# Optimization experiments

Hardware: AMD Instinct MI355X
Metric: run time of the kernel (lower is better)

Reference implementation:

```python
import jax, jax.numpy as jnp
import numpy as np

RADIUS = 0.1
NSAMPLE = 32
STRIDE = 4
EPS = 1e-5


def fps(p, M):
    # Furthest point sampling. p: [B, N, 3] -> idx [B, M] int32. First point is index 0.
    B, N, _ = p.shape

    def body(carry, _):
        dmin, last = carry
        lp = jnp.take_along_axis(p, last[:, None, None], axis=1)  # [B,1,3]
        d = jnp.sum((p - lp) ** 2, axis=-1)                       # [B,N]
        dmin = jnp.minimum(dmin, d)
        nxt = jnp.argmax(dmin, axis=-1).astype(jnp.int32)
        return (dmin, nxt), nxt

    first = jnp.zeros((B,), jnp.int32)
    dmin0 = jnp.full((B, N), jnp.inf, p.dtype)
    _, rest = jax.lax.scan(body, (dmin0, first), None, length=M - 1)
    return jnp.concatenate([first[None, :], rest], axis=0).T  # [B,M]


def ball_query(new_p, p, radius, K):
    # For each query, first K support indices with dist < radius (CUDA ballquery semantics:
    # pad with first found index; 0 if none). new_p [B,M,3], p [B,N,3] -> [B,M,K] int32.
    N = p.shape[1]
    d2 = (jnp.sum(new_p ** 2, -1)[:, :, None] + jnp.sum(p ** 2, -1)[:, None, :]
          - 2.0 * jnp.einsum('bmd,bnd->bmn', new_p, p))  # [B,M,N]
    scores = jnp.where(d2 < radius * radius,
                       jnp.arange(N, dtype=jnp.int32)[None, None, :], N)
    neg_vals, _ = jax.lax.top_k(-scores, K)  # K smallest scores, ascending
    idx = -neg_vals
    first = jnp.where(idx[..., :1] >= N, 0, idx[..., :1])
    return jnp.where(idx >= N, first, idx)


def bn(x, g, b):
    # BatchNorm (training-mode batch stats) over all dims except channel dim 1.
    axes = tuple(i for i in range(x.ndim) if i != 1)
    m = jnp.mean(x, axes, keepdims=True)
    v = jnp.var(x, axes, keepdims=True)
    shape = (1, -1) + (1,) * (x.ndim - 2)
    return g.reshape(shape) * (x - m) * jax.lax.rsqrt(v + EPS) + b.reshape(shape)


def setup_inputs() -> dict:
    key = jax.random.key(0)
    ks = jax.random.split(key, 6)
    B, N, C = 4, 8192, 64
    return {
        'p': jax.random.uniform(ks[0], (B, N, 3), jnp.float32),
        'f': jax.random.normal(ks[1], (B, C, N), jnp.float32),
        'w1': jax.random.normal(ks[2], (64, 3 + C), jnp.float32) * 0.05,
        'g1': jnp.ones((64,), jnp.float32),
        'b1': jnp.zeros((64,), jnp.float32),
        'w2': jax.random.normal(ks[3], (128, 64), jnp.float32) * 0.05,
        'g2': jnp.ones((128,), jnp.float32),
        'b2': jnp.zeros((128,), jnp.float32),
        'w_skip': jax.random.normal(ks[4], (128, C), jnp.float32) * 0.05,
        'b_skip': jnp.zeros((128,), jnp.float32),
    }


def reference(p, f, w1, g1, b1, w2, g2, b2, w_skip, b_skip):
    B, N, _ = p.shape
    C = f.shape[1]
    M = N // STRIDE
    idx = fps(p, M)                                                # [B,M]
    new_p = jnp.take_along_axis(p, idx[:, :, None], axis=1)        # [B,M,3]
    # residual branch: gather sampled features, 1x1 conv1d skip
    fi = jnp.take_along_axis(f, jnp.broadcast_to(idx[:, None, :], (B, C, M)), axis=2)
    identity = jnp.einsum('oc,bcm->bom', w_skip, fi) + b_skip[None, :, None]
    # ball-query grouping
    nidx = ball_query(new_p, p, RADIUS, NSAMPLE)                   # [B,M,K]
    flat = nidx.reshape(B, 1, M * NSAMPLE)
    pj = jnp.take_along_axis(p.transpose(0, 2, 1),
                             jnp.broadcast_to(flat, (B, 3, M * NSAMPLE)),
                             axis=2).reshape(B, 3, M, NSAMPLE)
    dp = pj - new_p.transpose(0, 2, 1)[:, :, :, None]              # [B,3,M,K]
    fj = jnp.take_along_axis(f, jnp.broadcast_to(flat, (B, C, M * NSAMPLE)),
                             axis=2).reshape(B, C, M, NSAMPLE)
    x = jnp.concatenate([dp, fj], axis=1)                          # [B,3+C,M,K]
    # conv-bn-relu, conv-bn (last block no act because use_res)
    x = jax.nn.relu(bn(jnp.einsum('oc,bcmk->bomk', w1, x), g1, b1))
    x = bn(jnp.einsum('oc,bcmk->bomk', w2, x), g2, b2)
    fout = jnp.max(x, axis=-1)                                     # [B,128,M]
    fout = jax.nn.relu(fout + identity)
    return new_p, fout, idx
```

## Files before the change

### kernel.cpp

```cpp
#include <hip/hip_runtime.h>
#include <math.h>

#define BB 4
#define NP 8192
#define CF 64
#define MQ 2048
#define KS 32

#define WS_G      0u
#define WS_NIDX   2097152u
#define WS_IDXI   2359296u
#define WS_ST1    2367488u
#define WS_ST2    2375680u
#define WS_SC1    2392064u
#define WS_SC2    2392192u
#define WS_MAXY2  2392448u

typedef float v2f __attribute__((ext_vector_type(2)));

#define FPS_T 256
#define FPS_NK 16

template <int CTRL>
__device__ __forceinline__ unsigned long long dpp_max_step(unsigned long long k) {
  int lo = (int)(unsigned)k;
  int hi = (int)(unsigned)(k >> 32);
  int slo = __builtin_amdgcn_update_dpp(0, lo, CTRL, 0xF, 0xF, true);
  int shi = __builtin_amdgcn_update_dpp(0, hi, CTRL, 0xF, 0xF, true);
  unsigned long long s =
      ((unsigned long long)(unsigned)shi << 32) | (unsigned long long)(unsigned)slo;
  return s > k ? s : k;
}

__global__ __launch_bounds__(256, 1) void fps_fused_kernel(
    const float* __restrict__ p, float* __restrict__ out, int* __restrict__ idx_i,
    const float* __restrict__ f, float* __restrict__ gout,
    const float* __restrict__ w1) {
#pragma clang fp contract(off)
  __shared__ __align__(16) char smem[NP * 16 + MQ * 4 + 2 * 4 * 8];
  int bx = blockIdx.x;
  int t = threadIdx.x;

  if (bx >= 4) {
    float (*tile)[65] = (float (*)[65])smem;
    float (*wlds)[68] = (float (*)[68])(smem + 16640);
    float* plds = (float*)(smem + 16640 + 17408);
    int tb = bx - 4;
    int b = tb >> 7;
    int n0 = (tb & 127) * 64;
    int cc = t >> 6;
    int nn = t & 63;
    #pragma unroll
    for (int r = 0; r < 16; ++r) {
      int c = cc * 16 + r;
      tile[c][nn] = f[((size_t)b * 64 + c) * NP + n0 + nn];
    }
    for (int i = t; i < 64 * 67; i += 256) {
      wlds[i / 67][i % 67] = w1[i];
    }
    if (t < 192) plds[t] = p[((size_t)b * NP + n0) * 3 + t];
    __syncthreads();
    int wv = t >> 6, lane = t & 63;
    float wreg[67];
    #pragma unroll
    for (int c = 0; c < 67; ++c) wreg[c] = wlds[lane][c];
    for (int q = 0; q < 16; ++q) {
      int pt = wv * 16 + q;
      float acc = wreg[0] * plds[pt * 3 + 0];
      acc += wreg[1] * plds[pt * 3 + 1];
      acc += wreg[2] * plds[pt * 3 + 2];
      #pragma unroll
      for (int c = 0; c < 64; ++c) acc += wreg[3 + c] * tile[c][pt];
      gout[((size_t)b * NP + n0 + pt) * 64 + lane] = acc;
    }
    return;
  }

  float4* sp4 = (float4*)smem;
  int* win = (int*)(smem + NP * 16);
  unsigned long long* wkey = (unsigned long long*)(smem + NP * 16 + MQ * 4);

  int b = bx;
  const float* pb = p + (size_t)b * NP * 3;
  float* out_newp = out;
  float* out_idxf = out + BB*MQ*3 + (size_t)BB*128*MQ;

  v2f px2[FPS_NK], py2[FPS_NK], pz2[FPS_NK];
  float dmn0[FPS_NK], dmn1[FPS_NK];
  #pragma unroll
  for (int k = 0; k < FPS_NK; ++k) {
    int i0 = (2*k) * FPS_T + t;
    int i1 = i0 + FPS_T;
    float x0 = pb[i0*3+0], y0 = pb[i0*3+1], z0 = pb[i0*3+2];
    float x1 = pb[i1*3+0], y1 = pb[i1*3+1], z1 = pb[i1*3+2];
    px2[k] = (v2f){x0, x1}; py2[k] = (v2f){y0, y1}; pz2[k] = (v2f){z0, z1};
    sp4[i0] = make_float4(x0, y0, z0, 0.0f);
    sp4[i1] = make_float4(x1, y1, z1, 0.0f);
    dmn0[k] = INFINITY; dmn1[k] = INFINITY;
  }
  if (t == 0) win[0] = 0;
  __syncthreads();
  float lx = sp4[0].x, ly = sp4[0].y, lz = sp4[0].z;
  unsigned nt = ~(unsigned)t;

  for (int j = 1; j < MQ; ++j) {
#pragma clang fp contract(off)
    v2f l2x = (v2f){lx, lx}, l2y = (v2f){ly, ly}, l2z = (v2f){lz, lz};
    float bv0 = -1.0f, bv1 = -1.0f;
    unsigned bk0 = 0u, bk1 = 0u;
    #pragma unroll
    for (int k = 0; k < FPS_NK; ++k) {
      v2f dx = px2[k] - l2x;
      v2f dy = py2[k] - l2y;
      v2f dz = pz2[k] - l2z;
      v2f dd = ((dx*dx) + (dy*dy)) + (dz*dz);
      float m0 = fminf(dmn0[k], dd.x);  dmn0[k] = m0;
      float m1 = fminf(dmn1[k], dd.y);  dmn1[k] = m1;
      bool g0 = m0 > bv0;
      bv0 = g0 ? m0 : bv0;
      bk0 = g0 ? (unsigned)k : bk0;
      bool g1 = m1 > bv1;
      bv1 = g1 ? m1 : bv1;
      bk1 = g1 ? (unsigned)k : bk1;
    }
    unsigned bn0 = nt - (bk0 << 9);
    unsigned bn1 = nt - (bk1 << 9) - 256u;
    unsigned long long k0 =
        ((unsigned long long)__float_as_uint(bv0) << 32) | (unsigned long long)bn0;
    unsigned long long k1 =
        ((unsigned long long)__float_as_uint(bv1) << 32) | (unsigned long long)bn1;
    unsigned long long key = k0 > k1 ? k0 : k1;
    key = dpp_max_step<0x111>(key);
    key = dpp_max_step<0x112>(key);
    key = dpp_max_step<0x114>(key);
    key = dpp_max_step<0x118>(key);
    key = dpp_max_step<0x142>(key);
    key = dpp_max_step<0x143>(key);
    if ((t & 63) == 63) wkey[(j & 1) * 4 + (t >> 6)] = key;
    __syncthreads();
    const ulonglong2* wk2 = (const ulonglong2*)(&wkey[(j & 1) * 4]);
    ulonglong2 ka = wk2[0];
    ulonglong2 kb = wk2[1];
    unsigned long long m0 = ka.x > ka.y ? ka.x : ka.y;
    unsigned long long m1 = kb.x > kb.y ? kb.x : kb.y;
    unsigned long long kw = m0 > m1 ? m0 : m1;
    int wi = (int)(~(unsigned)kw);
    float4 c = sp4[wi];
    lx = c.x; ly = c.y; lz = c.z;
    if (t == 0) win[j] = wi;
  }

  __syncthreads();
  #pragma unroll
  for (int k = 0; k < MQ / FPS_T; ++k) {
    int j = k * FPS_T + t;
    int wi = win[j];
    out_idxf[b*MQ + j] = (float)wi;
    idx_i[b*MQ + j] = wi;
    float4 c = sp4[wi];
    float* np_ = &out_newp[(size_t)(b*MQ + j) * 3];
    np_[0] = c.x; np_[1] = c.y; np_[2] = c.z;
  }
}

__global__ __launch_bounds__(256) void ballq_kernel(
    const float* __restrict__ p, const float* __restrict__ newp,
    int* __restrict__ nidx) {
  int qid = blockIdx.x * 4 + (threadIdx.x >> 6);
  int lane = threadIdx.x & 63;
  int b = qid >> 11;
  const float* pb = p + (size_t)b * NP * 3;
  float qx = newp[qid*3], qy = newp[qid*3+1], qz = newp[qid*3+2];
  float sq_q = __fadd_rn(__fadd_rn(__fmul_rn(qx,qx), __fmul_rn(qy,qy)), __fmul_rn(qz,qz));
  const float R2 = (float)(0.1 * 0.1);
  int found = 0, first = -1;
  int* outp = nidx + (size_t)qid * KS;
  for (int base = 0; base < NP; base += 64) {
    int n = base + lane;
    float x = pb[n*3], y = pb[n*3+1], z = pb[n*3+2];
    float sq_p = __fadd_rn(__fadd_rn(__fmul_rn(x,x), __fmul_rn(y,y)), __fmul_rn(z,z));
    float dot  = __fadd_rn(__fadd_rn(__fmul_rn(qx,x), __fmul_rn(qy,y)), __fmul_rn(qz,z));
    float d2   = __fadd_rn(__fadd_rn(sq_q, sq_p), __fmul_rn(-2.0f, dot));
    bool hit = d2 < R2;
    unsigned long long mask = __ballot(hit);
    if (mask) {
      if (first < 0) first = base + __builtin_ctzll(mask);
      int cnt = __popcll(mask);
      if (found < KS) {
        int rank = __popcll(mask & ((1ull << lane) - 1ull));
        if (hit && found + rank < KS) outp[found + rank] = n;
      }
      found += cnt;
      if (found >= KS) break;
    }
  }
  int fcl = found < KS ? found : KS;
  int padv = first < 0 ? 0 : first;
  if (lane >= fcl && lane < KS) outp[lane] = padv;
}

__global__ __launch_bounds__(256) void p1_kernel(
    const float* __restrict__ g, const float* __restrict__ newp,
    const float* __restrict__ w1, const int* __restrict__ nidx,
    float* __restrict__ stats1) {
  __shared__ float wbs[4][64], wbq[4][64];
  int wv = threadIdx.x >> 6, lane = threadIdx.x & 63;
  int qid = blockIdx.x * 4 + wv;
  int b = qid >> 11;
  int nv = (lane < KS) ? nidx[(size_t)qid * KS + lane] : 0;
  float qx = newp[qid*3], qy = newp[qid*3+1], qz = newp[qid*3+2];
  float w0 = w1[lane*67+0], w1c = w1[lane*67+1], w2c = w1[lane*67+2];
  float hq = w0*qx + w1c*qy + w2c*qz;
  float ss = 0.f, qq = 0.f;
  for (int kb = 0; kb < KS; kb += 8) {
    float gv[8];
    #pragma unroll
    for (int u = 0; u < 8; ++u) {
      int n = __shfl(nv, kb + u);
      gv[u] = g[((size_t)b * NP + n) * 64 + lane];
    }
    #pragma unroll
    for (int u = 0; u < 8; ++u) {
      float a = gv[u] - hq;
      ss += a; qq += a * a;
    }
  }
  wbs[wv][lane] = ss; wbq[wv][lane] = qq;
  __syncthreads();
  if (threadIdx.x < 64) {
    float s  = wbs[0][threadIdx.x] + wbs[1][threadIdx.x] + wbs[2][threadIdx.x] + wbs[3][threadIdx.x];
    float s2 = wbq[0][threadIdx.x] + wbq[1][threadIdx.x] + wbq[2][threadIdx.x] + wbq[3][threadIdx.x];
    int slice = blockIdx.x & 63;
    atomicAdd(&stats1[(slice*2+0)*64 + threadIdx.x], s);
    atomicAdd(&stats1[(slice*2+1)*64 + threadIdx.x], s2);
  }
}

__global__ void fin1_kernel(const float* __restrict__ stats1,
                            const float* __restrict__ g, const float* __restrict__ bb,
                            float* __restrict__ sc) {
  int o = threadIdx.x;
  float s = 0.f, q = 0.f;
  for (int sl = 0; sl < 64; ++sl) { s += stats1[(sl*2+0)*64+o]; q += stats1[(sl*2+1)*64+o]; }
  const float cnt = (float)(BB * MQ * KS);
  float mean = s / cnt;
  float var = q / cnt - mean * mean;
  float rstd = 1.0f / sqrtf(var + 1e-5f);
  float gs = g[o] * rstd;
  sc[o] = gs;
  sc[64+o] = bb[o] - mean * gs;
}

__global__ void fin2_kernel(const float* __restrict__ stats2,
                            const float* __restrict__ g, const float* __restrict__ bb,
                            float* __restrict__ sc) {
  int o = threadIdx.x;
  float s = 0.f, q = 0.f;
  for (int sl = 0; sl < 64; ++sl) { s += stats2[(sl*2+0)*128+o]; q += stats2[(sl*2+1)*128+o]; }
  const float cnt = (float)(BB * MQ * KS);
  float mean = s / cnt;
  float var = q / cnt - mean * mean;
  float rstd = 1.0f / sqrtf(var + 1e-5f);
  float gs = g[o] * rstd;
  sc[o] = gs;
  sc[128+o] = bb[o] - mean * gs;
}

__global__ __launch_bounds__(256) void p2_kernel(
    const float* __restrict__ g, const float* __restrict__ newp,
    const float* __restrict__ w1, const float* __restrict__ w2,
    const int* __restrict__ nidx, const float* __restrict__ sc1,
    float* __restrict__ stats2, float* __restrict__ maxy2) {
  __shared__ __align__(16) float xbuf[4][KS][68];
  __shared__ float wbs[4][128], wbq[4][128];
  int wv = threadIdx.x >> 6, lane = threadIdx.x & 63;
  int qid = blockIdx.x * 4 + wv;
  int b = qid >> 11;
  int nv = (lane < KS) ? nidx[(size_t)qid * KS + lane] : 0;
  float qx = newp[qid*3], qy = newp[qid*3+1], qz = newp[qid*3+2];
  float w0 = w1[lane*67+0], w1c = w1[lane*67+1], w2c = w1[lane*67+2];
  float hq = w0*qx + w1c*qy + w2c*qz;
  float s1v = sc1[lane], t1v = sc1[64 + lane];
  for (int kb = 0; kb < KS; kb += 8) {
    float gv[8];
    #pragma unroll
    for (int u = 0; u < 8; ++u) {
      int n = __shfl(nv, kb + u);
      gv[u] = g[((size_t)b * NP + n) * 64 + lane];
    }
    #pragma unroll
    for (int u = 0; u < 8; ++u) {
      float a = gv[u] - hq;
      float h = fmaxf(0.0f, fmaf(a, s1v, t1v));
      xbuf[wv][kb + u][lane] = h;
    }
  }
  __syncthreads();
  const float4* w2a = (const float4*)(w2 + (size_t)lane * 64);
  const float4* w2b = (const float4*)(w2 + (size_t)(lane + 64) * 64);
  float4 wra[16], wrb[16];
  #pragma unroll
  for (int c4 = 0; c4 < 16; ++c4) { wra[c4] = w2a[c4]; wrb[c4] = w2b[c4]; }
  float ss0 = 0.f, qq0 = 0.f, mx0 = -INFINITY;
  float ss1 = 0.f, qq1 = 0.f, mx1 = -INFINITY;
  for (int kk = 0; kk < KS; ++kk) {
    const float4* hr = (const float4*)(&xbuf[wv][kk][0]);
    float a0 = 0.f, a1 = 0.f;
    #pragma unroll
    for (int c4 = 0; c4 < 16; ++c4) {
      float4 h4 = hr[c4];
      float4 wa = wra[c4]; float4 wb = wrb[c4];
      a0 += wa.x*h4.x + wa.y*h4.y + wa.z*h4.z + wa.w*h4.w;
      a1 += wb.x*h4.x + wb.y*h4.y + wb.z*h4.z + wb.w*h4.w;
    }
    ss0 += a0; qq0 += a0*a0; mx0 = fmaxf(mx0, a0);
    ss1 += a1; qq1 += a1*a1; mx1 = fmaxf(mx1, a1);
  }
  maxy2[(size_t)qid * 128 + lane] = mx0;
  maxy2[(size_t)qid * 128 + 64 + lane] = mx1;
  wbs[wv][lane] = ss0; wbs[wv][64+lane] = ss1;
  wbq[wv][lane] = qq0; wbq[wv][64+lane] = qq1;
  __syncthreads();
  if (threadIdx.x < 128) {
    float s  = wbs[0][threadIdx.x] + wbs[1][threadIdx.x] + wbs[2][threadIdx.x] + wbs[3][threadIdx.x];
    float s2 = wbq[0][threadIdx.x] + wbq[1][threadIdx.x] + wbq[2][threadIdx.x] + wbq[3][threadIdx.x];
    int slice = blockIdx.x & 63;
    atomicAdd(&stats2[(slice*2+0)*128 + threadIdx.x], s);
    atomicAdd(&stats2[(slice*2+1)*128 + threadIdx.x], s2);
  }
}

__global__ __launch_bounds__(256) void p3_kernel(
    const float* __restrict__ f, const int* __restrict__ idx_i,
    const float* __restrict__ w_skip, const float* __restrict__ b_skip,
    const float* __restrict__ sc2, const float* __restrict__ maxy2,
    float* __restrict__ outf) {
  __shared__ __align__(16) float flds[4][64];
  int wv = threadIdx.x >> 6, lane = threadIdx.x & 63;
  int qid = blockIdx.x * 4 + wv;
  int b = qid >> 11, m = qid & (MQ - 1);
  int n = idx_i[qid];
  flds[wv][lane] = f[((size_t)b * 64 + lane) * NP + n];
  const float4* f4 = (const float4*)(&flds[wv][0]);
  const float4* wa = (const float4*)(w_skip + (size_t)lane * 64);
  const float4* wb = (const float4*)(w_skip + (size_t)(lane + 64) * 64);
  float a0 = b_skip[lane], a1 = b_skip[lane + 64];
  #pragma unroll
  for (int c4 = 0; c4 < 16; ++c4) {
    float4 x = f4[c4]; float4 u = wa[c4]; float4 v = wb[c4];
    a0 += u.x*x.x + u.y*x.y + u.z*x.z + u.w*x.w;
    a1 += v.x*x.x + v.y*x.y + v.z*x.z + v.w*x.w;
  }
  float v0 = maxy2[(size_t)qid * 128 + lane];
  float v1 = maxy2[(size_t)qid * 128 + 64 + lane];
  float r0 = fmaxf(0.0f, fmaf(v0, sc2[lane],      sc2[128 + lane])      + a0);
  float r1 = fmaxf(0.0f, fmaf(v1, sc2[lane + 64], sc2[128 + lane + 64]) + a1);
  outf[((size_t)b * 128 + lane) * MQ + m] = r0;
  outf[((size_t)b * 128 + lane + 64) * MQ + m] = r1;
}

extern "C" void kernel_launch(void* const* d_in, const int* in_sizes, int n_in,
                              void* d_out, int out_size, void* d_ws, size_t ws_size,
                              hipStream_t stream) {
  (void)in_sizes; (void)n_in; (void)out_size; (void)ws_size;
  const float* p   = (const float*)d_in[0];
  const float* f   = (const float*)d_in[1];
  const float* w1  = (const float*)d_in[2];
  const float* g1  = (const float*)d_in[3];
  const float* b1  = (const float*)d_in[4];
  const float* w2  = (const float*)d_in[5];
  const float* g2  = (const float*)d_in[6];
  const float* b2  = (const float*)d_in[7];
  const float* wsk = (const float*)d_in[8];
  const float* bsk = (const float*)d_in[9];
  float* out = (float*)d_out;
  float* wsf = (float*)d_ws;

  float* gbuf  = wsf + WS_G;
  int*   nidx  = (int*)(wsf + WS_NIDX);
  int*   idxi  = (int*)(wsf + WS_IDXI);
  float* st1   = wsf + WS_ST1;
  float* st2   = wsf + WS_ST2;
  float* sc1   = wsf + WS_SC1;
  float* sc2   = wsf + WS_SC2;
  float* maxy2 = wsf + WS_MAXY2;

  float* out_newp = out;
  float* out_f    = out + BB*MQ*3;

  (void)hipMemsetAsync(st1, 0, (8192 + 16384) * sizeof(float), stream);

  fps_fused_kernel<<<4 + 512, FPS_T, 0, stream>>>(p, out, idxi, f, gbuf, w1);
  ballq_kernel<<<BB*MQ/4, 256, 0, stream>>>(p, out_newp, nidx);
  p1_kernel<<<BB*MQ/4, 256, 0, stream>>>(gbuf, out_newp, w1, nidx, st1);
  fin1_kernel<<<1, 64, 0, stream>>>(st1, g1, b1, sc1);
  p2_kernel<<<BB*MQ/4, 256, 0, stream>>>(gbuf, out_newp, w1, w2, nidx, sc1, st2, maxy2);
  fin2_kernel<<<1, 128, 0, stream>>>(st2, g2, b2, sc2);
  p3_kernel<<<BB*MQ/4, 256, 0, stream>>>(f, idxi, wsk, bsk, sc2, maxy2, out_f);
}
```

Measured before the change: 1.906 ms.

## Fold BN finalize into consumer kernels, prefetch ball-query points, pad LDS weight rows

Result: no change. 1.914 ms (+0.4%).

```diff
diff --git a/kernel.cpp b/kernel.cpp
--- a/kernel.cpp
+++ b/kernel.cpp
@@ -12,8 +12,6 @@
 #define WS_IDXI   2359296u
 #define WS_ST1    2367488u
 #define WS_ST2    2375680u
-#define WS_SC1    2392064u
-#define WS_SC2    2392192u
 #define WS_MAXY2  2392448u
 
 typedef float v2f __attribute__((ext_vector_type(2)));
@@ -43,8 +41,8 @@
 
   if (bx >= 4) {
     float (*tile)[65] = (float (*)[65])smem;
-    float (*wlds)[68] = (float (*)[68])(smem + 16640);
-    float* plds = (float*)(smem + 16640 + 17408);
+    float (*wlds)[69] = (float (*)[69])(smem + 16640);
+    float* plds = (float*)(smem + 16640 + 17664);
     int tb = bx - 4;
     int b = tb >> 7;
     int n0 = (tb & 127) * 64;
@@ -175,9 +173,11 @@
   const float R2 = (float)(0.1 * 0.1);
   int found = 0, first = -1;
   int* outp = nidx + (size_t)qid * KS;
+  float x = pb[lane*3], y = pb[lane*3+1], z = pb[lane*3+2];
   for (int base = 0; base < NP; base += 64) {
+    int nf = (base + 64 < NP) ? (base + 64 + lane) : lane;
+    float xn = pb[nf*3], yn = pb[nf*3+1], zn = pb[nf*3+2];
     int n = base + lane;
-    float x = pb[n*3], y = pb[n*3+1], z = pb[n*3+2];
     float sq_p = __fadd_rn(__fadd_rn(__fmul_rn(x,x), __fmul_rn(y,y)), __fmul_rn(z,z));
     float dot  = __fadd_rn(__fadd_rn(__fmul_rn(qx,x), __fmul_rn(qy,y)), __fmul_rn(qz,z));
     float d2   = __fadd_rn(__fadd_rn(sq_q, sq_p), __fmul_rn(-2.0f, dot));
@@ -193,6 +193,7 @@
       found += cnt;
       if (found >= KS) break;
     }
+    x = xn; y = yn; z = zn;
   }
   int fcl = found < KS ? found : KS;
   int padv = first < 0 ? 0 : first;
@@ -236,51 +237,39 @@
   }
 }
 
-__global__ void fin1_kernel(const float* __restrict__ stats1,
-                            const float* __restrict__ g, const float* __restrict__ bb,
-                            float* __restrict__ sc) {
-  int o = threadIdx.x;
-  float s = 0.f, q = 0.f;
-  for (int sl = 0; sl < 64; ++sl) { s += stats1[(sl*2+0)*64+o]; q += stats1[(sl*2+1)*64+o]; }
-  const float cnt = (float)(BB * MQ * KS);
-  float mean = s / cnt;
-  float var = q / cnt - mean * mean;
-  float rstd = 1.0f / sqrtf(var + 1e-5f);
-  float gs = g[o] * rstd;
-  sc[o] = gs;
-  sc[64+o] = bb[o] - mean * gs;
-}
-
-__global__ void fin2_kernel(const float* __restrict__ stats2,
-                            const float* __restrict__ g, const float* __restrict__ bb,
-                            float* __restrict__ sc) {
-  int o = threadIdx.x;
-  float s = 0.f, q = 0.f;
-  for (int sl = 0; sl < 64; ++sl) { s += stats2[(sl*2+0)*128+o]; q += stats2[(sl*2+1)*128+o]; }
-  const float cnt = (float)(BB * MQ * KS);
-  float mean = s / cnt;
-  float var = q / cnt - mean * mean;
-  float rstd = 1.0f / sqrtf(var + 1e-5f);
-  float gs = g[o] * rstd;
-  sc[o] = gs;
-  sc[128+o] = bb[o] - mean * gs;
-}
-
 __global__ __launch_bounds__(256) void p2_kernel(
     const float* __restrict__ g, const float* __restrict__ newp,
     const float* __restrict__ w1, const float* __restrict__ w2,
-    const int* __restrict__ nidx, const float* __restrict__ sc1,
+    const int* __restrict__ nidx, const float* __restrict__ stats1,
+    const float* __restrict__ g1, const float* __restrict__ b1,
     float* __restrict__ stats2, float* __restrict__ maxy2) {
   __shared__ __align__(16) float xbuf[4][KS][68];
   __shared__ float wbs[4][128], wbq[4][128];
+  __shared__ float scb[128];
   int wv = threadIdx.x >> 6, lane = threadIdx.x & 63;
   int qid = blockIdx.x * 4 + wv;
   int b = qid >> 11;
+  if (threadIdx.x < 64) {
+    int o = threadIdx.x;
+    float s = 0.f, q = 0.f;
+    for (int sl = 0; sl < 64; ++sl) {
+      s += stats1[(sl*2+0)*64 + o];
+      q += stats1[(sl*2+1)*64 + o];
+    }
+    const float cnt = (float)(BB * MQ * KS);
+    float mean = s / cnt;
+    float var = q / cnt - mean * mean;
+    float rstd = 1.0f / sqrtf(var + 1e-5f);
+    float gs = g1[o] * rstd;
+    scb[o] = gs;
+    scb[64 + o] = b1[o] - mean * gs;
+  }
   int nv = (lane < KS) ? nidx[(size_t)qid * KS + lane] : 0;
   float qx = newp[qid*3], qy = newp[qid*3+1], qz = newp[qid*3+2];
   float w0 = w1[lane*67+0], w1c = w1[lane*67+1], w2c = w1[lane*67+2];
   float hq = w0*qx + w1c*qy + w2c*qz;
-  float s1v = sc1[lane], t1v = sc1[64 + lane];
+  __syncthreads();
+  float s1v = scb[lane], t1v = scb[64 + lane];
   for (int kb = 0; kb < KS; kb += 8) {
     float gv[8];
     #pragma unroll
@@ -333,14 +322,32 @@
 __global__ __launch_bounds__(256) void p3_kernel(
     const float* __restrict__ f, const int* __restrict__ idx_i,
     const float* __restrict__ w_skip, const float* __restrict__ b_skip,
-    const float* __restrict__ sc2, const float* __restrict__ maxy2,
-    float* __restrict__ outf) {
+    const float* __restrict__ stats2,
+    const float* __restrict__ g2, const float* __restrict__ b2,
+    const float* __restrict__ maxy2, float* __restrict__ outf) {
   __shared__ __align__(16) float flds[4][64];
+  __shared__ float scb[256];
   int wv = threadIdx.x >> 6, lane = threadIdx.x & 63;
   int qid = blockIdx.x * 4 + wv;
   int b = qid >> 11, m = qid & (MQ - 1);
   int n = idx_i[qid];
+  if (threadIdx.x < 128) {
+    int o = threadIdx.x;
+    float s = 0.f, q = 0.f;
+    for (int sl = 0; sl < 64; ++sl) {
+      s += stats2[(sl*2+0)*128 + o];
+      q += stats2[(sl*2+1)*128 + o];
+    }
+    const float cnt = (float)(BB * MQ * KS);
+    float mean = s / cnt;
+    float var = q / cnt - mean * mean;
+    float rstd = 1.0f / sqrtf(var + 1e-5f);
+    float gs = g2[o] * rstd;
+    scb[o] = gs;
+    scb[128 + o] = b2[o] - mean * gs;
+  }
   flds[wv][lane] = f[((size_t)b * 64 + lane) * NP + n];
+  __syncthreads();
   const float4* f4 = (const float4*)(&flds[wv][0]);
   const float4* wa = (const float4*)(w_skip + (size_t)lane * 64);
   const float4* wb = (const float4*)(w_skip + (size_t)(lane + 64) * 64);
@@ -353,8 +360,8 @@
   }
   float v0 = maxy2[(size_t)qid * 128 + lane];
   float v1 = maxy2[(size_t)qid * 128 + 64 + lane];
-  float r0 = fmaxf(0.0f, fmaf(v0, sc2[lane],      sc2[128 + lane])      + a0);
-  float r1 = fmaxf(0.0f, fmaf(v1, sc2[lane + 64], sc2[128 + lane + 64]) + a1);
+  float r0 = fmaxf(0.0f, fmaf(v0, scb[lane],      scb[128 + lane])      + a0);
+  float r1 = fmaxf(0.0f, fmaf(v1, scb[lane + 64], scb[128 + lane + 64]) + a1);
   outf[((size_t)b * 128 + lane) * MQ + m] = r0;
   outf[((size_t)b * 128 + lane + 64) * MQ + m] = r1;
 }
@@ -381,8 +388,6 @@
   int*   idxi  = (int*)(wsf + WS_IDXI);
   float* st1   = wsf + WS_ST1;
   float* st2   = wsf + WS_ST2;
-  float* sc1   = wsf + WS_SC1;
-  float* sc2   = wsf + WS_SC2;
   float* maxy2 = wsf + WS_MAXY2;
 
   float* out_newp = out;
@@ -393,8 +398,6 @@
   fps_fused_kernel<<<4 + 512, FPS_T, 0, stream>>>(p, out, idxi, f, gbuf, w1);
   ballq_kernel<<<BB*MQ/4, 256, 0, stream>>>(p, out_newp, nidx);
   p1_kernel<<<BB*MQ/4, 256, 0, stream>>>(gbuf, out_newp, w1, nidx, st1);
-  fin1_kernel<<<1, 64, 0, stream>>>(st1, g1, b1, sc1);
-  p2_kernel<<<BB*MQ/4, 256, 0, stream>>>(gbuf, out_newp, w1, w2, nidx, sc1, st2, maxy2);
-  fin2_kernel<<<1, 128, 0, stream>>>(st2, g2, b2, sc2);
-  p3_kernel<<<BB*MQ/4, 256, 0, stream>>>(f, idxi, wsk, bsk, sc2, maxy2, out_f);
-}
+  p2_kernel<<<BB*MQ/4, 256, 0, stream>>>(gbuf, out_newp, w1, w2, nidx, st1, g1, b1, st2, maxy2);
+  p3_kernel<<<BB*MQ/4, 256, 0, stream>>>(f, idxi, wsk, bsk, st2, g2, b2, maxy2, out_f);
+}
```
